# Optimization experiments

Measured on AMD Instinct MI355X. Metric: run time of the kernel, lower is better.

The kernel has to match this reference:

```python
import jax, jax.numpy as jnp
import numpy as np

ANCHORS = jnp.array([[10,14],[23,27],[37,58],[81,82],[135,169],[344,319]], jnp.float32)
ANCHOR_MASK = [[3,4,5],[1,2,3]]
NUM_CLASSES = 80
IMAGE_HW = (1080.0, 1920.0)   # (h, w) of source image
MAX_BOXES = 20
SCORE_THR = 0.6
IOU_THR = 0.5
NEG = jnp.float32(-1e30)      # sentinel for suppressed scores


def decode_layer(feats, anchors_l):
    """yolo_head + yolo_correct_boxes for one detection head. feats: [1,H,W,3*(C+5)]."""
    _, H, W, _ = feats.shape
    f = feats.reshape(H, W, 3, NUM_CLASSES + 5)
    gy, gx = jnp.meshgrid(jnp.arange(H), jnp.arange(W), indexing='ij')
    grid = jnp.stack([gx, gy], axis=-1).astype(f.dtype)[:, :, None, :]  # [H,W,1,2] (x,y)
    input_hw = jnp.array([H * 32.0, W * 32.0], f.dtype)                 # network input (h,w)
    # decode
    box_xy = (jax.nn.sigmoid(f[..., :2]) + grid) / jnp.array([W, H], f.dtype)
    box_wh = jnp.exp(f[..., 2:4]) * anchors_l / input_hw[::-1]          # anchors_l: [3,2] (w,h)
    conf = jax.nn.sigmoid(f[..., 4:5])
    probs = jax.nn.sigmoid(f[..., 5:])
    # letterbox correction (yolo_correct_boxes)
    box_yx = box_xy[..., ::-1]
    box_hw = box_wh[..., ::-1]
    image_hw = jnp.array(IMAGE_HW, f.dtype)
    new_shape = jnp.round(image_hw * jnp.min(input_hw / image_hw))
    offset = (input_hw - new_shape) / 2.0 / input_hw
    scale = input_hw / new_shape
    box_yx = (box_yx - offset) * scale
    box_hw = box_hw * scale
    mins = box_yx - box_hw / 2.0
    maxes = box_yx + box_hw / 2.0
    boxes = jnp.concatenate([mins, maxes], axis=-1) * jnp.concatenate([image_hw, image_hw])
    return boxes.reshape(-1, 4), (conf * probs).reshape(-1, NUM_CLASSES)


def nms_per_class(boxes, scores_c):
    """Greedy NMS for one class. boxes: [N,4] (ymin,xmin,ymax,xmax), scores_c: [N].
    Fixed-size (jit-friendly) equivalent of boolean_mask + tf.image.non_max_suppression:
    below-threshold scores are masked to NEG; output is padded to MAX_BOXES slots."""
    areas = (boxes[:, 2] - boxes[:, 0]) * (boxes[:, 3] - boxes[:, 1])
    s0 = jnp.where(scores_c >= SCORE_THR, scores_c, NEG)

    def body(s, _):
        i = jnp.argmax(s)
        valid = s[i] > NEG / 2
        b = boxes[i]
        yx1 = jnp.maximum(b[:2], boxes[:, :2])
        yx2 = jnp.minimum(b[2:], boxes[:, 2:])
        inter = jnp.prod(jnp.clip(yx2 - yx1, 0.0), axis=-1)
        union = areas[i] + areas - inter
        iou = jnp.where(union > 0, inter / union, 0.0)
        s_next = jnp.where((iou > IOU_THR) & valid, NEG, s)
        s_next = s_next.at[i].set(NEG)
        return s_next, (i, valid)

    _, (idx, valid) = jax.lax.scan(body, s0, None, length=MAX_BOXES)
    sel_boxes = boxes[idx] * valid[:, None].astype(boxes.dtype)   # [MAX_BOXES,4]
    sel_scores = scores_c[idx] * valid.astype(scores_c.dtype)     # [MAX_BOXES]
    return sel_boxes, sel_scores, valid


def setup_inputs() -> dict:
    key = jax.random.key(0)
    k0, k1 = jax.random.split(key)
    feats0 = jax.random.normal(k0, (1, 96, 96, 3 * (NUM_CLASSES + 5)), jnp.float32)
    feats1 = jax.random.normal(k1, (1, 192, 192, 3 * (NUM_CLASSES + 5)), jnp.float32)
    return {"feats0": feats0, "feats1": feats1}


def reference(feats0, feats1):
    b0, s0 = decode_layer(feats0, ANCHORS[jnp.array(ANCHOR_MASK[0])])
    b1, s1 = decode_layer(feats1, ANCHORS[jnp.array(ANCHOR_MASK[1])])
    boxes = jnp.concatenate([b0, b1], axis=0)      # [N,4]
    scores = jnp.concatenate([s0, s1], axis=0)     # [N,80]
    sel_b, sel_s, valid = jax.vmap(nms_per_class, in_axes=(None, 1))(boxes, scores)
    classes = jnp.broadcast_to(jnp.arange(NUM_CLASSES, dtype=jnp.int32)[:, None],
                               (NUM_CLASSES, MAX_BOXES))
    classes = jnp.where(valid, classes, -1).reshape(-1)
    return sel_b.reshape(-1, 4), sel_s.reshape(-1), classes
```

## Files before the change

kernel.cpp:

```cpp
#include <hip/hip_runtime.h>

#define NCLS 80
#define MAXB 20
#define N0 27648
#define N1 110592
#define NTOT (N0 + N1)
#define CAP 8192
#define DT 512
#define DSTAGE 3072
#define CNT_STRIDE 16
#define NMS_T 1024
#define NB 256
#define TARGET 64
#define SCAP 256

__device__ __forceinline__ float sigf(float x) {
    return 1.0f / (1.0f + expf(-x));
}

__device__ __forceinline__ unsigned wave_max_bcast(unsigned x) {
    unsigned t;
    t = (unsigned)__builtin_amdgcn_update_dpp((int)x, (int)x, 0x111, 0xF, 0xF, false); x = x > t ? x : t;
    t = (unsigned)__builtin_amdgcn_update_dpp((int)x, (int)x, 0x112, 0xF, 0xF, false); x = x > t ? x : t;
    t = (unsigned)__builtin_amdgcn_update_dpp((int)x, (int)x, 0x114, 0xF, 0xF, false); x = x > t ? x : t;
    t = (unsigned)__builtin_amdgcn_update_dpp((int)x, (int)x, 0x118, 0xF, 0xF, false); x = x > t ? x : t;
    t = (unsigned)__builtin_amdgcn_update_dpp((int)x, (int)x, 0x142, 0xF, 0xF, false); x = x > t ? x : t;
    t = (unsigned)__builtin_amdgcn_update_dpp((int)x, (int)x, 0x143, 0xF, 0xF, false); x = x > t ? x : t;
    return (unsigned)__builtin_amdgcn_readlane((int)x, 63);
}

__device__ __forceinline__ unsigned wave_min_bcast(unsigned x) {
    unsigned t;
    t = (unsigned)__builtin_amdgcn_update_dpp((int)x, (int)x, 0x111, 0xF, 0xF, false); x = x < t ? x : t;
    t = (unsigned)__builtin_amdgcn_update_dpp((int)x, (int)x, 0x112, 0xF, 0xF, false); x = x < t ? x : t;
    t = (unsigned)__builtin_amdgcn_update_dpp((int)x, (int)x, 0x114, 0xF, 0xF, false); x = x < t ? x : t;
    t = (unsigned)__builtin_amdgcn_update_dpp((int)x, (int)x, 0x118, 0xF, 0xF, false); x = x < t ? x : t;
    t = (unsigned)__builtin_amdgcn_update_dpp((int)x, (int)x, 0x142, 0xF, 0xF, false); x = x < t ? x : t;
    t = (unsigned)__builtin_amdgcn_update_dpp((int)x, (int)x, 0x143, 0xF, 0xF, false); x = x < t ? x : t;
    return (unsigned)__builtin_amdgcn_readlane((int)x, 63);
}

__device__ __forceinline__ unsigned wave_incl_scan(unsigned x) {
    x += (unsigned)__builtin_amdgcn_update_dpp(0, (int)x, 0x111, 0xF, 0xF, false);
    x += (unsigned)__builtin_amdgcn_update_dpp(0, (int)x, 0x112, 0xF, 0xF, false);
    x += (unsigned)__builtin_amdgcn_update_dpp(0, (int)x, 0x114, 0xF, 0xF, false);
    x += (unsigned)__builtin_amdgcn_update_dpp(0, (int)x, 0x118, 0xF, 0xF, false);
    x += (unsigned)__builtin_amdgcn_update_dpp(0, (int)x, 0x142, 0xA, 0xF, false);
    x += (unsigned)__builtin_amdgcn_update_dpp(0, (int)x, 0x143, 0xC, 0xF, false);
    return x;
}

__global__ __launch_bounds__(DT) void decode_kernel(
    const float* __restrict__ feats0, const float* __restrict__ feats1,
    float4* __restrict__ boxes, uint2* __restrict__ cands,
    int* __restrict__ counts)
{
    __shared__ unsigned p_gi[DT];
    __shared__ float    p_conf[DT];
    __shared__ int s_npass;
    __shared__ float    s_esc[DSTAGE];
    __shared__ unsigned s_ent[DSTAGE];
    __shared__ unsigned short s_lp[DSTAGE];
    __shared__ int s_n;
    __shared__ int s_cnt[NCLS];
    __shared__ int s_base[NCLS];

    int tid = threadIdx.x;
    if (tid == 0) { s_npass = 0; s_n = 0; }
    if (tid < NCLS) s_cnt[tid] = 0;
    __syncthreads();

    const float* feats;
    int S, base, i;
    float aw0, ah0, aw1, ah1, aw2, ah2;
    if (blockIdx.x < N0 / DT) {
        feats = feats0; S = 96; base = 0;
        i = blockIdx.x * DT + tid;
        aw0 = 81.0f;  ah0 = 82.0f;  aw1 = 135.0f; ah1 = 169.0f; aw2 = 344.0f; ah2 = 319.0f;
    } else {
        feats = feats1; S = 192; base = N0;
        i = (blockIdx.x - N0 / DT) * DT + tid;
        aw0 = 23.0f;  ah0 = 27.0f;  aw1 = 37.0f;  ah1 = 58.0f;  aw2 = 81.0f;  ah2 = 82.0f;
    }

    const float* f = feats + (size_t)i * 85;
    float4 head = *reinterpret_cast<const float4*>(f);
    float sconf = sigf(f[4]);
    if (sconf >= 0.6f) {
        int sl = atomicAdd(&s_npass, 1);
        p_gi[sl] = (unsigned)(base + i);
        p_conf[sl] = sconf;

        int a = i % 3;
        int cell = i / 3;
        int gx = cell % S;
        int gy = cell / S;

        float Sf = (float)S;
        float inpf = Sf * 32.0f;
        float aw = (a == 0) ? aw0 : ((a == 1) ? aw1 : aw2);
        float ah = (a == 0) ? ah0 : ((a == 1) ? ah1 : ah2);

        float x = (sigf(head.x) + (float)gx) / Sf;
        float y = (sigf(head.y) + (float)gy) / Sf;
        float w = expf(head.z) * aw / inpf;
        float h = expf(head.w) * ah / inpf;

        const float OFF = 0.21875f;
        const float SC  = 3072.0f / 1728.0f;
        float yy = (y - OFF) * SC;
        float hh = h * SC;

        boxes[base + i] = make_float4((yy - hh * 0.5f) * 1080.0f,
                                      (x  - w  * 0.5f) * 1920.0f,
                                      (yy + hh * 0.5f) * 1080.0f,
                                      (x  + w  * 0.5f) * 1920.0f);
    }
    __syncthreads();

    int npass = s_npass;

    int tot = npass * (NCLS / 4);
    for (int wk0 = tid; wk0 < tot; wk0 += DT * 4) {
        float4   pv[4];
        unsigned gi4[4];
        float    cf[4];
        int      g4[4];
#pragma unroll
        for (int j = 0; j < 4; ++j) {
            int wk = wk0 + j * DT;
            if (wk < tot) {
                int sl = wk / (NCLS / 4);
                int g  = wk - sl * (NCLS / 4);
                gi4[j] = p_gi[sl];
                cf[j] = p_conf[sl];
                g4[j] = g;
                pv[j] = *reinterpret_cast<const float4*>(
                    feats + (size_t)(gi4[j] - (unsigned)base) * 85 + 5 + g * 4);
            }
        }
#pragma unroll
        for (int j = 0; j < 4; ++j) {
            int wk = wk0 + j * DT;
            if (wk < tot) {
#pragma unroll
                for (int q = 0; q < 4; ++q) {
                    float pj = (q == 0) ? pv[j].x : (q == 1) ? pv[j].y
                             : (q == 2) ? pv[j].z : pv[j].w;
                    float s = cf[j] * sigf(pj);
                    if (s >= 0.6f) {
                        int c = g4[j] * 4 + q;
                        int e = atomicAdd(&s_n, 1);
                        int lp = atomicAdd(&s_cnt[c], 1);
                        if (e < DSTAGE) {
                            s_esc[e] = s;
                            s_ent[e] = gi4[j] | ((unsigned)c << 18);
                            s_lp[e] = (unsigned short)lp;
                        }
                    }
                }
            }
        }
    }
    __syncthreads();

    int n = s_n < DSTAGE ? s_n : DSTAGE;

    if (tid < NCLS) {
        int k = s_cnt[tid];
        s_base[tid] = (k > 0) ? atomicAdd(&counts[tid * CNT_STRIDE], k) : 0;
    }
    __syncthreads();

    for (int e = tid; e < n; e += DT) {
        unsigned ent = s_ent[e];
        int c = ent >> 18;
        int pos = s_base[c] + (int)s_lp[e];
        if (pos < CAP)
            cands[(size_t)c * CAP + pos] =
                make_uint2(__float_as_uint(s_esc[e]), ent & 0x3FFFFu);
    }
}

__global__ __launch_bounds__(NMS_T) void nms_kernel(
    const float4* __restrict__ boxes, const uint2* __restrict__ cands,
    const int* __restrict__ counts, float* __restrict__ out)
{
    __shared__ int s_hist[NB];
    __shared__ int s_tau;
    __shared__ int s_m;
    __shared__ float4   s_cbox[SCAP];
    __shared__ unsigned s_csc[SCAP];
    __shared__ unsigned s_cix[SCAP];
    __shared__ unsigned char s_alive[CAP];

    int c = blockIdx.x;
    int tid = threadIdx.x;

    int cnt = counts[c * CNT_STRIDE];
    if (cnt > CAP) cnt = CAP;

    const uint2* cl = cands + (size_t)c * CAP;

    if (tid < NB) s_hist[tid] = 0;
    if (tid == 0) s_m = 0;
    __syncthreads();

    for (int e0 = tid; e0 < cnt; e0 += NMS_T * 4) {
        unsigned sc4[4];
#pragma unroll
        for (int j = 0; j < 4; ++j) {
            int e = e0 + j * NMS_T;
            if (e < cnt) sc4[j] = cl[e].x;
        }
#pragma unroll
        for (int j = 0; j < 4; ++j) {
            int e = e0 + j * NMS_T;
            if (e < cnt)
                atomicAdd(&s_hist[(sc4[j] - 0x3F199999u) >> 15], 1);
        }
    }
    __syncthreads();

    if (tid < 64) {
        unsigned acc = 0;
        bool found = false;
        for (int ch = NB / 64 - 1; ch >= 0 && !found; --ch) {
            unsigned h = (unsigned)s_hist[ch * 64 + tid];
            unsigned incl = wave_incl_scan(h);
            unsigned total = (unsigned)__builtin_amdgcn_readlane((int)incl, 63);
            bool ok = acc + (total - incl + h) >= (unsigned)TARGET;
            unsigned long long mk = __ballot(ok);
            if (mk) {
                if (tid == 0) s_tau = ch * 64 + (63 - __builtin_clzll(mk));
                found = true;
            }
            acc += total;
        }
        if (!found && tid == 0) s_tau = 0;
    }
    __syncthreads();

    int tau = s_tau;
    for (int e0 = tid; e0 < cnt; e0 += NMS_T * 4) {
        uint2 v4[4];
#pragma unroll
        for (int j = 0; j < 4; ++j) {
            int e = e0 + j * NMS_T;
            if (e < cnt) v4[j] = cl[e];
        }
#pragma unroll
        for (int j = 0; j < 4; ++j) {
            int e = e0 + j * NMS_T;
            if (e < cnt && (int)((v4[j].x - 0x3F199999u) >> 15) >= tau) {
                int p = atomicAdd(&s_m, 1);
                if (p < SCAP) {
                    s_csc[p] = v4[j].x;
                    s_cix[p] = v4[j].y;
                    s_cbox[p] = boxes[v4[j].y];
                }
            }
        }
    }
    __syncthreads();

    if (tid >= 64) return;

    int lane = tid;
    int m = s_m;
    bool need_fb = (m > SCAP);
    if (m > SCAP) m = SCAP;

    float* ob  = out;
    float* os  = out + 6400;
    float* ocl = out + 8000;

    int sel = 0;

    if (!need_fb) {
        unsigned scu[4], ixu[4];
        float4 bx[4];
        float  ar[4];
#pragma unroll
        for (int k = 0; k < 4; ++k) {
            int e = lane + k * 64;
            scu[k] = 0u; ixu[k] = 0xFFFFFFFFu;
            bx[k] = make_float4(0.f, 0.f, 0.f, 0.f);
            ar[k] = 0.f;
            if (e < m) {
                scu[k] = s_csc[e];
                ixu[k] = s_cix[e];
                bx[k] = s_cbox[e];
                ar[k] = (bx[k].z - bx[k].x) * (bx[k].w - bx[k].y);
            }
        }

        for (; sel < MAXB; ++sel) {
            unsigned lm = 0u;
#pragma unroll
            for (int k = 0; k < 4; ++k) lm = lm > scu[k] ? lm : scu[k];
            unsigned smax = wave_max_bcast(lm);
            if (smax == 0u) {
                if (m < cnt) need_fb = true;
                break;
            }
            unsigned li = 0xFFFFFFFFu;
#pragma unroll
            for (int k = 0; k < 4; ++k)
                if (scu[k] == smax && ixu[k] < li) li = ixu[k];
            unsigned bidx = wave_min_bcast(li);

            bool has = false;
            float4 ob_ = make_float4(0.f, 0.f, 0.f, 0.f);
#pragma unroll
            for (int k = 0; k < 4; ++k)
                if (scu[k] == smax && ixu[k] == bidx) { ob_ = bx[k]; has = true; }
            unsigned long long mk = __ballot(has);
            int src = __ffsll((long long)mk) - 1;
            float4 sb;
            sb.x = __int_as_float(__builtin_amdgcn_readlane(__float_as_int(ob_.x), src));
            sb.y = __int_as_float(__builtin_amdgcn_readlane(__float_as_int(ob_.y), src));
            sb.z = __int_as_float(__builtin_amdgcn_readlane(__float_as_int(ob_.z), src));
            sb.w = __int_as_float(__builtin_amdgcn_readlane(__float_as_int(ob_.w), src));
            float area_s = (sb.z - sb.x) * (sb.w - sb.y);

            if (lane == 0) {
                int o = c * MAXB + sel;
                ob[o * 4 + 0] = sb.x; ob[o * 4 + 1] = sb.y;
                ob[o * 4 + 2] = sb.z; ob[o * 4 + 3] = sb.w;
                os[o]  = __uint_as_float(smax);
                ocl[o] = (float)c;
            }

#pragma unroll
            for (int k = 0; k < 4; ++k) {
                if (scu[k] != 0u) {
                    float y1 = fmaxf(sb.x, bx[k].x);
                    float x1 = fmaxf(sb.y, bx[k].y);
                    float y2 = fminf(sb.z, bx[k].z);
                    float x2 = fminf(sb.w, bx[k].w);
                    float inter = fmaxf(y2 - y1, 0.f) * fmaxf(x2 - x1, 0.f);
                    float un = area_s + ar[k] - inter;
                    float iou = (un > 0.f) ? (inter / un) : 0.f;
                    if (iou > 0.5f || ixu[k] == bidx) scu[k] = 0u;
                }
            }
        }
    }

    if (need_fb) {
        for (int e = lane; e < cnt; e += 64) s_alive[e] = 1;
        sel = 0;
        for (; sel < MAXB; ++sel) {
            unsigned bs = 0u, bi = 0xFFFFFFFFu;
            for (int e = lane; e < cnt; e += 64) {
                if (s_alive[e]) {
                    uint2 v = cl[e];
                    if (v.x > bs || (v.x == bs && v.y < bi)) { bs = v.x; bi = v.y; }
                }
            }
            unsigned smax = wave_max_bcast(bs);
            if (smax == 0u) break;
            unsigned li = (bs == smax) ? bi : 0xFFFFFFFFu;
            unsigned bidx = wave_min_bcast(li);

            float4 sb = boxes[bidx];
            float area_s = (sb.z - sb.x) * (sb.w - sb.y);

            if (lane == 0) {
                int o = c * MAXB + sel;
                ob[o * 4 + 0] = sb.x; ob[o * 4 + 1] = sb.y;
                ob[o * 4 + 2] = sb.z; ob[o * 4 + 3] = sb.w;
                os[o]  = __uint_as_float(smax);
                ocl[o] = (float)c;
            }

            for (int e = lane; e < cnt; e += 64) {
                if (s_alive[e]) {
                    uint2 v = cl[e];
                    float4 cb = boxes[v.y];
                    float y1 = fmaxf(sb.x, cb.x);
                    float x1 = fmaxf(sb.y, cb.y);
                    float y2 = fminf(sb.z, cb.z);
                    float x2 = fminf(sb.w, cb.w);
                    float inter = fmaxf(y2 - y1, 0.f) * fmaxf(x2 - x1, 0.f);
                    float area_c = (cb.z - cb.x) * (cb.w - cb.y);
                    float un = area_s + area_c - inter;
                    float iou = (un > 0.f) ? (inter / un) : 0.f;
                    if (iou > 0.5f || v.y == bidx) s_alive[e] = 0;
                }
            }
        }
    }

    for (int q = sel + lane; q < MAXB; q += 64) {
        int o = c * MAXB + q;
        ob[o * 4 + 0] = 0.0f; ob[o * 4 + 1] = 0.0f;
        ob[o * 4 + 2] = 0.0f; ob[o * 4 + 3] = 0.0f;
        os[o]  = 0.0f;
        ocl[o] = -1.0f;
    }
}

extern "C" void kernel_launch(void* const* d_in, const int* in_sizes, int n_in,
                              void* d_out, int out_size, void* d_ws, size_t ws_size,
                              hipStream_t stream) {
    const float* feats0 = (const float*)d_in[0];
    const float* feats1 = (const float*)d_in[1];
    float* out = (float*)d_out;

    char* ws = (char*)d_ws;
    float4* boxes  = (float4*)ws;
    int*    counts = (int*)(ws + 2211840);
    uint2*  cands  = (uint2*)(ws + 2211840 + 8192);

    hipMemsetAsync(counts, 0, NCLS * CNT_STRIDE * sizeof(int), stream);

    decode_kernel<<<NTOT / DT, DT, 0, stream>>>(feats0, feats1, boxes, cands, counts);

    nms_kernel<<<NCLS, NMS_T, 0, stream>>>(boxes, cands, counts, out);
}
```

Measured before the change: 44.82 us.

## Fuse decode and NMS into one kernel with a global completion counter

Merges the decode and per-class NMS kernels into a single launch. Every block increments a global done counter, and the first 80 blocks spin until all 270 blocks have finished decoding before running NMS for their class. This removes one kernel launch and the gap between launches. NMS now runs with 512 threads instead of 1024, and the spin-wait depends on all blocks being co-resident or scheduled, with the waiting blocks holding CUs that later blocks might need.

```diff
diff --git a/kernel.cpp b/kernel.cpp
--- a/kernel.cpp
+++ b/kernel.cpp
@@ -7,9 +7,9 @@
 #define NTOT (N0 + N1)
 #define CAP 8192
 #define DT 512
+#define NBLK (NTOT / DT)
 #define DSTAGE 3072
 #define CNT_STRIDE 16
-#define NMS_T 1024
 #define NB 256
 #define TARGET 64
 #define SCAP 256
@@ -50,10 +50,11 @@
     return x;
 }
 
-__global__ __launch_bounds__(DT) void decode_kernel(
+__global__ __launch_bounds__(DT) void fused_kernel(
     const float* __restrict__ feats0, const float* __restrict__ feats1,
     float4* __restrict__ boxes, uint2* __restrict__ cands,
-    int* __restrict__ counts)
+    int* __restrict__ counts, int* __restrict__ done,
+    float* __restrict__ out)
 {
     __shared__ unsigned p_gi[DT];
     __shared__ float    p_conf[DT];
@@ -64,8 +65,16 @@
     __shared__ int s_n;
     __shared__ int s_cnt[NCLS];
     __shared__ int s_base[NCLS];
+    __shared__ int s_hist[NB];
+    __shared__ int s_tau;
+    __shared__ int s_m;
+    __shared__ float4   s_cbox[SCAP];
+    __shared__ unsigned s_csc[SCAP];
+    __shared__ unsigned s_cix[SCAP];
+    __shared__ unsigned char s_alive[CAP];
 
     int tid = threadIdx.x;
+    int blk = blockIdx.x;
     if (tid == 0) { s_npass = 0; s_n = 0; }
     if (tid < NCLS) s_cnt[tid] = 0;
     __syncthreads();
@@ -73,13 +82,13 @@
     const float* feats;
     int S, base, i;
     float aw0, ah0, aw1, ah1, aw2, ah2;
-    if (blockIdx.x < N0 / DT) {
+    if (blk < N0 / DT) {
         feats = feats0; S = 96; base = 0;
-        i = blockIdx.x * DT + tid;
+        i = blk * DT + tid;
         aw0 = 81.0f;  ah0 = 82.0f;  aw1 = 135.0f; ah1 = 169.0f; aw2 = 344.0f; ah2 = 319.0f;
     } else {
         feats = feats1; S = 192; base = N0;
-        i = (blockIdx.x - N0 / DT) * DT + tid;
+        i = (blk - N0 / DT) * DT + tid;
         aw0 = 23.0f;  ah0 = 27.0f;  aw1 = 37.0f;  ah1 = 58.0f;  aw2 = 81.0f;  ah2 = 82.0f;
     }
 
@@ -180,22 +189,22 @@
             cands[(size_t)c * CAP + pos] =
                 make_uint2(__float_as_uint(s_esc[e]), ent & 0x3FFFFu);
     }
-}
-
-__global__ __launch_bounds__(NMS_T) void nms_kernel(
-    const float4* __restrict__ boxes, const uint2* __restrict__ cands,
-    const int* __restrict__ counts, float* __restrict__ out)
-{
-    __shared__ int s_hist[NB];
-    __shared__ int s_tau;
-    __shared__ int s_m;
-    __shared__ float4   s_cbox[SCAP];
-    __shared__ unsigned s_csc[SCAP];
-    __shared__ unsigned s_cix[SCAP];
-    __shared__ unsigned char s_alive[CAP];
-
-    int c = blockIdx.x;
-    int tid = threadIdx.x;
+
+    __threadfence();
+    __syncthreads();
+    if (tid == 0) {
+        __hip_atomic_fetch_add(done, 1, __ATOMIC_ACQ_REL, __HIP_MEMORY_SCOPE_AGENT);
+        if (blk < NCLS) {
+            while (__hip_atomic_load(done, __ATOMIC_ACQUIRE,
+                                     __HIP_MEMORY_SCOPE_AGENT) < NBLK)
+                __builtin_amdgcn_s_sleep(2);
+        }
+    }
+    if (blk >= NCLS) return;
+    __syncthreads();
+    __threadfence();
+
+    int c = blk;
 
     int cnt = counts[c * CNT_STRIDE];
     if (cnt > CAP) cnt = CAP;
@@ -206,16 +215,16 @@
     if (tid == 0) s_m = 0;
     __syncthreads();
 
-    for (int e0 = tid; e0 < cnt; e0 += NMS_T * 4) {
+    for (int e0 = tid; e0 < cnt; e0 += DT * 4) {
         unsigned sc4[4];
 #pragma unroll
         for (int j = 0; j < 4; ++j) {
-            int e = e0 + j * NMS_T;
+            int e = e0 + j * DT;
             if (e < cnt) sc4[j] = cl[e].x;
         }
 #pragma unroll
         for (int j = 0; j < 4; ++j) {
-            int e = e0 + j * NMS_T;
+            int e = e0 + j * DT;
             if (e < cnt)
                 atomicAdd(&s_hist[(sc4[j] - 0x3F199999u) >> 15], 1);
         }
@@ -242,16 +251,16 @@
     __syncthreads();
 
     int tau = s_tau;
-    for (int e0 = tid; e0 < cnt; e0 += NMS_T * 4) {
+    for (int e0 = tid; e0 < cnt; e0 += DT * 4) {
         uint2 v4[4];
 #pragma unroll
         for (int j = 0; j < 4; ++j) {
-            int e = e0 + j * NMS_T;
+            int e = e0 + j * DT;
             if (e < cnt) v4[j] = cl[e];
         }
 #pragma unroll
         for (int j = 0; j < 4; ++j) {
-            int e = e0 + j * NMS_T;
+            int e = e0 + j * DT;
             if (e < cnt && (int)((v4[j].x - 0x3F199999u) >> 15) >= tau) {
                 int p = atomicAdd(&s_m, 1);
                 if (p < SCAP) {
@@ -412,11 +421,11 @@
     char* ws = (char*)d_ws;
     float4* boxes  = (float4*)ws;
     int*    counts = (int*)(ws + 2211840);
+    int*    done   = (int*)(ws + 2211840 + 5120);
     uint2*  cands  = (uint2*)(ws + 2211840 + 8192);
 
-    hipMemsetAsync(counts, 0, NCLS * CNT_STRIDE * sizeof(int), stream);
-
-    decode_kernel<<<NTOT / DT, DT, 0, stream>>>(feats0, feats1, boxes, cands, counts);
-
-    nms_kernel<<<NCLS, NMS_T, 0, stream>>>(boxes, cands, counts, out);
-}
+    hipMemsetAsync(ws + 2211840, 0, 8192, stream);
+
+    fused_kernel<<<NBLK, DT, 0, stream>>>(feats0, feats1, boxes, cands,
+                                          counts, done, out);
+}
```

Result: slower. 128.9 us (+187.5%).
